# Optimization experiments

Measured on AMD Instinct MI355X. Metric: run time of the kernel, lower is better.

The kernel has to match this reference:

```python
import jax, jax.numpy as jnp
import numpy as np

N_NODES = 50000
N_EDGES = 800000
IN_F = 128
OUT_F = 128

def setup_inputs() -> dict:
    key = jax.random.key(0)
    k1, k2, k3, k4, k5, k6 = jax.random.split(key, 6)
    x = jax.random.normal(k1, (N_NODES, IN_F), dtype=jnp.float32)
    edge_row = jax.random.randint(k2, (N_EDGES,), 0, N_NODES, dtype=jnp.int32)
    edge_col = jax.random.randint(k3, (N_EDGES,), 0, N_NODES, dtype=jnp.int32)
    edge_val = jax.random.uniform(k4, (N_EDGES,), dtype=jnp.float32)
    stdv = 1.0 / np.sqrt(OUT_F)
    weight = jax.random.uniform(k5, (IN_F, OUT_F), minval=-stdv, maxval=stdv, dtype=jnp.float32)
    bias_param = jax.random.uniform(k6, (OUT_F,), minval=-stdv, maxval=stdv, dtype=jnp.float32)
    return {"x": x, "edge_row": edge_row, "edge_col": edge_col,
            "edge_val": edge_val, "weight": weight, "bias_param": bias_param}

def reference(x, edge_row, edge_col, edge_val, weight, bias_param):
    # support = X @ W  (dense GEMM)
    support = jnp.matmul(x, weight)                      # [N, out_f]
    # out = spmm(adj, support): gather source rows, scale by edge value,
    # scatter-add into destination rows (COO SpMM)
    msgs = edge_val[:, None] * support[edge_col]         # [E, out_f]
    out = jax.ops.segment_sum(msgs, edge_row, num_segments=N_NODES)
    return out + bias_param
```

## Files before the change

kernel.cpp:

```cpp
#include <hip/hip_runtime.h>

#define IN_F 128
#define OUT_F 128
#define BROWS 64
#define BCAP  2048
#define NBMAX 1024

typedef __attribute__((ext_vector_type(8))) short short8;
typedef __attribute__((ext_vector_type(4))) float floatx4;

__device__ __forceinline__ short f2bf(float f) {
  union { float f; unsigned u; } v; v.f = f;
  unsigned u = v.u;
  unsigned r = (u + 0x7fffu + ((u >> 16) & 1u)) >> 16;
  return (short)r;
}
__device__ __forceinline__ float bflo(unsigned u) { return __uint_as_float(u << 16); }
__device__ __forceinline__ float bfhi(unsigned u) { return __uint_as_float(u & 0xffff0000u); }

__global__ __launch_bounds__(256) void prep_wt(const float* __restrict__ w,
                                               short* __restrict__ wt) {
  int i = blockIdx.x * 256 + threadIdx.x;
  int n = i >> 7, k = i & 127;
  wt[i] = f2bf(w[k * 128 + n]);
}

__global__ __launch_bounds__(256) void gemm_mfma(const float* __restrict__ x,
                                                 const short* __restrict__ wt,
                                                 unsigned short* __restrict__ sup,
                                                 int n) {
  const int w    = threadIdx.x >> 6;
  const int lane = threadIdx.x & 63;
  const int m    = lane & 15;
  const int q    = lane >> 4;
  const int row  = blockIdx.x * 64 + w * 16 + m;

  floatx4 acc[8];
#pragma unroll
  for (int t = 0; t < 8; ++t) acc[t] = (floatx4)(0.f);

#pragma unroll
  for (int kk = 0; kk < 4; ++kk) {
    short8 a;
    if (row < n) {
      const float4* px = (const float4*)(x + (size_t)row * IN_F + kk * 32 + q * 8);
      float4 lo = px[0], hi = px[1];
      a[0] = f2bf(lo.x); a[1] = f2bf(lo.y); a[2] = f2bf(lo.z); a[3] = f2bf(lo.w);
      a[4] = f2bf(hi.x); a[5] = f2bf(hi.y); a[6] = f2bf(hi.z); a[7] = f2bf(hi.w);
    } else {
      a = (short8)(0);
    }
#pragma unroll
    for (int t = 0; t < 8; ++t) {
      short8 b = *(const short8*)(wt + (size_t)(16 * t + m) * 128 + kk * 32 + q * 8);
      acc[t] = __builtin_amdgcn_mfma_f32_16x16x32_bf16(a, b, acc[t], 0, 0, 0);
    }
  }

#pragma unroll
  for (int r = 0; r < 4; ++r) {
    int row_out = blockIdx.x * 64 + w * 16 + q * 4 + r;
    if (row_out < n) {
#pragma unroll
      for (int t = 0; t < 8; ++t) {
        sup[(size_t)row_out * OUT_F + 16 * t + m] = (unsigned short)f2bf(acc[t][r]);
      }
    }
  }
}

__global__ __launch_bounds__(256) void init_cursor(int* __restrict__ cursor, int nb) {
  int b = blockIdx.x * 256 + threadIdx.x;
  if (b < nb) cursor[b] = b * BCAP;
}

__global__ __launch_bounds__(256) void bin_edges(const int* __restrict__ erow,
                                                 const int* __restrict__ ecol,
                                                 const float* __restrict__ eval_,
                                                 int* __restrict__ cursor,
                                                 int2* __restrict__ slab,
                                                 int n_edges, int nb) {
  __shared__ int lhist[NBMAX];
  const int t = threadIdx.x;
  for (int b = t; b < nb; b += 256) lhist[b] = 0;
  __syncthreads();

  const int base = blockIdx.x * 4096;
  int meta[16], col[16]; float val[16];
#pragma unroll
  for (int i = 0; i < 16; ++i) {
    int e = base + i * 256 + t;
    meta[i] = -1;
    if (e < n_edges) {
      int r  = erow[e];
      col[i] = ecol[e];
      val[i] = eval_[e];
      int b = r >> 6, rl = r & 63;
      int rank = atomicAdd(&lhist[b], 1);
      meta[i] = (b << 18) | (rl << 12) | rank;
    }
  }
  __syncthreads();

  for (int b = t; b < nb; b += 256) {
    int c = lhist[b];
    lhist[b] = c ? atomicAdd(&cursor[b], c) : 0;
  }
  __syncthreads();

#pragma unroll
  for (int i = 0; i < 16; ++i) {
    if (meta[i] >= 0) {
      int b = meta[i] >> 18, rl = (meta[i] >> 12) & 63, rank = meta[i] & 0xfff;
      int pos = lhist[b] + rank;
      if (pos < (b + 1) * BCAP)
        slab[pos] = make_int2(col[i] | (rl << 16), __float_as_int(val[i]));
    }
  }
}

__global__ __launch_bounds__(256) void spmm_sorted(const int* __restrict__ cursor,
                                                   const int2* __restrict__ slab,
                                                   const uint4* __restrict__ supv,
                                                   const float* __restrict__ bias,
                                                   float* __restrict__ out,
                                                   int n_nodes) {
  __shared__ int2 srec[BCAP];
  __shared__ int  roff[BROWS + 1];
  __shared__ int  rcur[BROWS];
  const int t = threadIdx.x, b = blockIdx.x;
  const int start = b * BCAP;
  const int cnt = min(cursor[b] - start, BCAP);
  const int w = t >> 6, lane = t & 63;

  if (t < BROWS) rcur[t] = 0;
  __syncthreads();
  for (int i = t; i < cnt; i += 256)
    atomicAdd(&rcur[(slab[start + i].x >> 16) & 63], 1);
  __syncthreads();
  if (w == 0) {
    int inc = rcur[lane];
    #pragma unroll
    for (int d = 1; d < 64; d <<= 1) {
      int u = __shfl_up(inc, d);
      if (lane >= d) inc += u;
    }
    roff[lane + 1] = inc;
    if (lane == 0) roff[0] = 0;
  }
  __syncthreads();
  if (t < BROWS) rcur[t] = roff[t];
  __syncthreads();
  for (int i = t; i < cnt; i += 256) {
    int2 r = slab[start + i];
    int p = atomicAdd(&rcur[(r.x >> 16) & 63], 1);
    srec[p] = r;
  }
  __syncthreads();

  const int g = lane >> 4, s = lane & 15;
  const float4* bp = (const float4*)bias + s * 2;
  const float4 b0 = bp[0], b1 = bp[1];

  for (int it = 0; it < 4; ++it) {
    const int rl = w * 16 + it * 4 + g;
    const int s0 = roff[rl];
    const int c  = roff[rl + 1] - s0;
    int mx = max(c, __shfl_xor(c, 16));
    mx = max(mx, __shfl_xor(mx, 32));

    float a0 = 0.f, a1 = 0.f, a2 = 0.f, a3 = 0.f,
          a4 = 0.f, a5 = 0.f, a6 = 0.f, a7 = 0.f;

    int2 rec0 = make_int2(0, 0), rec1 = make_int2(0, 0);
    if (0 < c) rec0 = srec[s0];
    if (1 < c) rec1 = srec[s0 + 1];
    uint4 sv0 = supv[(size_t)(rec0.x & 0xffff) * 16 + s];
    uint4 sv1 = supv[(size_t)(rec1.x & 0xffff) * 16 + s];

    for (int j = 0; j < mx; ++j) {
      int2 rec2 = make_int2(0, 0);
      if (j + 2 < c) rec2 = srec[s0 + j + 2];
      uint4 sv2 = supv[(size_t)(rec2.x & 0xffff) * 16 + s];
      float v = (j < c) ? __int_as_float(rec0.y) : 0.f;
      a0 = fmaf(v, bflo(sv0.x), a0);
      a1 = fmaf(v, bfhi(sv0.x), a1);
      a2 = fmaf(v, bflo(sv0.y), a2);
      a3 = fmaf(v, bfhi(sv0.y), a3);
      a4 = fmaf(v, bflo(sv0.z), a4);
      a5 = fmaf(v, bfhi(sv0.z), a5);
      a6 = fmaf(v, bflo(sv0.w), a6);
      a7 = fmaf(v, bfhi(sv0.w), a7);
      rec0 = rec1; rec1 = rec2; sv0 = sv1; sv1 = sv2;
    }

    const int row = b * BROWS + rl;
    if (row < n_nodes) {
      float4* op = (float4*)(out + (size_t)row * OUT_F + s * 8);
      op[0] = make_float4(a0 + b0.x, a1 + b0.y, a2 + b0.z, a3 + b0.w);
      op[1] = make_float4(a4 + b1.x, a5 + b1.y, a6 + b1.z, a7 + b1.w);
    }
  }
}

extern "C" void kernel_launch(void* const* d_in, const int* in_sizes, int n_in,
                              void* d_out, int out_size, void* d_ws, size_t ws_size,
                              hipStream_t stream) {
  const float* x     = (const float*)d_in[0];
  const int*   erow  = (const int*)d_in[1];
  const int*   ecol  = (const int*)d_in[2];
  const float* eval_ = (const float*)d_in[3];
  const float* w     = (const float*)d_in[4];
  const float* bias  = (const float*)d_in[5];
  float* out = (float*)d_out;

  const int n_nodes = in_sizes[0] / IN_F;
  const int n_edges = in_sizes[1];
  const int nb = (n_nodes + BROWS - 1) / BROWS;

  char* ws = (char*)d_ws;
  size_t off = 0;
  auto carve = [&](size_t bytes) { void* p = ws + off; off = (off + bytes + 255) & ~(size_t)255; return p; };
  unsigned short* sup = (unsigned short*)carve((size_t)n_nodes * OUT_F * sizeof(unsigned short));
  short* wt           = (short*)carve((size_t)IN_F * OUT_F * sizeof(short));
  int*   cursor       = (int*)  carve((size_t)nb * sizeof(int));
  int2*  slab         = (int2*) carve((size_t)nb * BCAP * sizeof(int2));

  prep_wt<<<(IN_F * OUT_F) / 256, 256, 0, stream>>>(w, wt);
  gemm_mfma<<<(n_nodes + 63) / 64, 256, 0, stream>>>(x, wt, sup, n_nodes);
  init_cursor<<<(nb + 255) / 256, 256, 0, stream>>>(cursor, nb);
  bin_edges<<<(n_edges + 4095) / 4096, 256, 0, stream>>>(erow, ecol, eval_, cursor, slab,
                                                         n_edges, nb);
  spmm_sorted<<<nb, 256, 0, stream>>>(cursor, slab, (const uint4*)sup, bias, out, n_nodes);
}
```

Measured before the change: 152.0 us.

## Fuse all stages into one persistent cooperative kernel with grid syncs

Merges weight prep, GEMM, cursor init, edge binning and SpMM into a single cooperative persistent kernel separated by grid.sync. The GEMM tiles and edge-binning chunks run concurrently in one work loop. Row buckets shrink to 32 rows with a smaller per-bucket capacity and 2048-edge chunks. This removes several kernel launches and lets the GEMM overlap with binning. In exchange it adds grid-wide barriers, extra shared-memory use from the combined buffers that may lower occupancy, and a tighter bucket capacity (mean about 512 edges per bucket, cap 768) that could overflow and silently drop edges.

```diff
diff --git a/kernel.cpp b/kernel.cpp
--- a/kernel.cpp
+++ b/kernel.cpp
@@ -1,10 +1,14 @@
 #include <hip/hip_runtime.h>
+#include <hip/hip_cooperative_groups.h>
+
+namespace cg = cooperative_groups;
 
 #define IN_F 128
 #define OUT_F 128
-#define BROWS 64
-#define BCAP  2048
-#define NBMAX 1024
+#define BROWS 32
+#define BCAP  768
+#define CHUNK 2048
+#define NBMAX 2048
 
 typedef __attribute__((ext_vector_type(8))) short short8;
 typedef __attribute__((ext_vector_type(4))) float floatx4;
@@ -18,188 +22,184 @@
 __device__ __forceinline__ float bflo(unsigned u) { return __uint_as_float(u << 16); }
 __device__ __forceinline__ float bfhi(unsigned u) { return __uint_as_float(u & 0xffff0000u); }
 
-__global__ __launch_bounds__(256) void prep_wt(const float* __restrict__ w,
-                                               short* __restrict__ wt) {
-  int i = blockIdx.x * 256 + threadIdx.x;
-  int n = i >> 7, k = i & 127;
-  wt[i] = f2bf(w[k * 128 + n]);
-}
-
-__global__ __launch_bounds__(256) void gemm_mfma(const float* __restrict__ x,
-                                                 const short* __restrict__ wt,
-                                                 unsigned short* __restrict__ sup,
-                                                 int n) {
-  const int w    = threadIdx.x >> 6;
-  const int lane = threadIdx.x & 63;
-  const int m    = lane & 15;
-  const int q    = lane >> 4;
-  const int row  = blockIdx.x * 64 + w * 16 + m;
-
-  floatx4 acc[8];
-#pragma unroll
-  for (int t = 0; t < 8; ++t) acc[t] = (floatx4)(0.f);
-
-#pragma unroll
-  for (int kk = 0; kk < 4; ++kk) {
-    short8 a;
-    if (row < n) {
-      const float4* px = (const float4*)(x + (size_t)row * IN_F + kk * 32 + q * 8);
-      float4 lo = px[0], hi = px[1];
-      a[0] = f2bf(lo.x); a[1] = f2bf(lo.y); a[2] = f2bf(lo.z); a[3] = f2bf(lo.w);
-      a[4] = f2bf(hi.x); a[5] = f2bf(hi.y); a[6] = f2bf(hi.z); a[7] = f2bf(hi.w);
-    } else {
-      a = (short8)(0);
-    }
-#pragma unroll
-    for (int t = 0; t < 8; ++t) {
-      short8 b = *(const short8*)(wt + (size_t)(16 * t + m) * 128 + kk * 32 + q * 8);
-      acc[t] = __builtin_amdgcn_mfma_f32_16x16x32_bf16(a, b, acc[t], 0, 0, 0);
-    }
-  }
-
-#pragma unroll
-  for (int r = 0; r < 4; ++r) {
-    int row_out = blockIdx.x * 64 + w * 16 + q * 4 + r;
-    if (row_out < n) {
-#pragma unroll
-      for (int t = 0; t < 8; ++t) {
-        sup[(size_t)row_out * OUT_F + 16 * t + m] = (unsigned short)f2bf(acc[t][r]);
-      }
-    }
-  }
-}
-
-__global__ __launch_bounds__(256) void init_cursor(int* __restrict__ cursor, int nb) {
-  int b = blockIdx.x * 256 + threadIdx.x;
-  if (b < nb) cursor[b] = b * BCAP;
-}
-
-__global__ __launch_bounds__(256) void bin_edges(const int* __restrict__ erow,
-                                                 const int* __restrict__ ecol,
-                                                 const float* __restrict__ eval_,
-                                                 int* __restrict__ cursor,
-                                                 int2* __restrict__ slab,
-                                                 int n_edges, int nb) {
-  __shared__ int lhist[NBMAX];
-  const int t = threadIdx.x;
-  for (int b = t; b < nb; b += 256) lhist[b] = 0;
-  __syncthreads();
-
-  const int base = blockIdx.x * 4096;
-  int meta[16], col[16]; float val[16];
-#pragma unroll
-  for (int i = 0; i < 16; ++i) {
-    int e = base + i * 256 + t;
-    meta[i] = -1;
-    if (e < n_edges) {
-      int r  = erow[e];
-      col[i] = ecol[e];
-      val[i] = eval_[e];
-      int b = r >> 6, rl = r & 63;
-      int rank = atomicAdd(&lhist[b], 1);
-      meta[i] = (b << 18) | (rl << 12) | rank;
-    }
-  }
-  __syncthreads();
-
-  for (int b = t; b < nb; b += 256) {
-    int c = lhist[b];
-    lhist[b] = c ? atomicAdd(&cursor[b], c) : 0;
-  }
-  __syncthreads();
-
-#pragma unroll
-  for (int i = 0; i < 16; ++i) {
-    if (meta[i] >= 0) {
-      int b = meta[i] >> 18, rl = (meta[i] >> 12) & 63, rank = meta[i] & 0xfff;
-      int pos = lhist[b] + rank;
-      if (pos < (b + 1) * BCAP)
-        slab[pos] = make_int2(col[i] | (rl << 16), __float_as_int(val[i]));
-    }
-  }
-}
-
-__global__ __launch_bounds__(256) void spmm_sorted(const int* __restrict__ cursor,
-                                                   const int2* __restrict__ slab,
-                                                   const uint4* __restrict__ supv,
-                                                   const float* __restrict__ bias,
-                                                   float* __restrict__ out,
-                                                   int n_nodes) {
+__global__ void fused(const float* __restrict__ x,
+                      const int* __restrict__ erow,
+                      const int* __restrict__ ecol,
+                      const float* __restrict__ eval_,
+                      const float* __restrict__ w,
+                      const float* __restrict__ bias,
+                      short* __restrict__ wt,
+                      int* __restrict__ cursor,
+                      int2* __restrict__ slab,
+                      unsigned short* __restrict__ sup,
+                      float* __restrict__ out,
+                      int n_nodes, int n_edges, int nb, int n_tiles, int n_chunks) {
+  __shared__ int  lhist[NBMAX];
   __shared__ int2 srec[BCAP];
   __shared__ int  roff[BROWS + 1];
   __shared__ int  rcur[BROWS];
-  const int t = threadIdx.x, b = blockIdx.x;
-  const int start = b * BCAP;
-  const int cnt = min(cursor[b] - start, BCAP);
-  const int w = t >> 6, lane = t & 63;
-
-  if (t < BROWS) rcur[t] = 0;
-  __syncthreads();
-  for (int i = t; i < cnt; i += 256)
-    atomicAdd(&rcur[(slab[start + i].x >> 16) & 63], 1);
-  __syncthreads();
-  if (w == 0) {
-    int inc = rcur[lane];
-    #pragma unroll
-    for (int d = 1; d < 64; d <<= 1) {
-      int u = __shfl_up(inc, d);
-      if (lane >= d) inc += u;
-    }
-    roff[lane + 1] = inc;
-    if (lane == 0) roff[0] = 0;
+  cg::grid_group grid = cg::this_grid();
+  const int t = threadIdx.x;
+  const int wv = t >> 6, lane = t & 63;
+  const int G = gridDim.x;
+
+  for (int i = blockIdx.x * 256 + t; i < IN_F * OUT_F; i += G * 256) {
+    int nn = i >> 7, k = i & 127;
+    wt[i] = f2bf(w[k * OUT_F + nn]);
   }
-  __syncthreads();
-  if (t < BROWS) rcur[t] = roff[t];
-  __syncthreads();
-  for (int i = t; i < cnt; i += 256) {
-    int2 r = slab[start + i];
-    int p = atomicAdd(&rcur[(r.x >> 16) & 63], 1);
-    srec[p] = r;
+  for (int i = blockIdx.x * 256 + t; i < nb; i += G * 256) cursor[i] = i * BCAP;
+  grid.sync();
+
+  for (int u = blockIdx.x; u < n_tiles + n_chunks; u += G) {
+    if (u < n_tiles) {
+      const int m = lane & 15, q = lane >> 4;
+      const int row = u * 64 + wv * 16 + m;
+#pragma unroll
+      for (int half = 0; half < 2; ++half) {
+        floatx4 acc[4];
+#pragma unroll
+        for (int i2 = 0; i2 < 4; ++i2) acc[i2] = (floatx4)(0.f);
+#pragma unroll
+        for (int kk = 0; kk < 4; ++kk) {
+          short8 a;
+          if (row < n_nodes) {
+            const float4* px = (const float4*)(x + (size_t)row * IN_F + kk * 32 + q * 8);
+            float4 lo = px[0], hi = px[1];
+            a[0] = f2bf(lo.x); a[1] = f2bf(lo.y); a[2] = f2bf(lo.z); a[3] = f2bf(lo.w);
+            a[4] = f2bf(hi.x); a[5] = f2bf(hi.y); a[6] = f2bf(hi.z); a[7] = f2bf(hi.w);
+          } else {
+            a = (short8)(0);
+          }
+#pragma unroll
+          for (int t4 = 0; t4 < 4; ++t4) {
+            int ncol = half * 64 + 16 * t4 + m;
+            short8 bfr = *(const short8*)(wt + (size_t)ncol * IN_F + kk * 32 + q * 8);
+            acc[t4] = __builtin_amdgcn_mfma_f32_16x16x32_bf16(a, bfr, acc[t4], 0, 0, 0);
+          }
+        }
+#pragma unroll
+        for (int r = 0; r < 4; ++r) {
+          int row_out = u * 64 + wv * 16 + q * 4 + r;
+          if (row_out < n_nodes) {
+#pragma unroll
+            for (int t4 = 0; t4 < 4; ++t4)
+              sup[(size_t)row_out * OUT_F + half * 64 + 16 * t4 + m] =
+                  (unsigned short)f2bf(acc[t4][r]);
+          }
+        }
+      }
+    } else {
+      const int C = u - n_tiles;
+      for (int i = t; i < nb; i += 256) lhist[i] = 0;
+      __syncthreads();
+      const int base = C * CHUNK;
+      int meta[CHUNK / 256]; int col8[CHUNK / 256]; float val8[CHUNK / 256];
+#pragma unroll
+      for (int i = 0; i < CHUNK / 256; ++i) {
+        int e = base + i * 256 + t;
+        meta[i] = -1;
+        if (e < n_edges) {
+          int r  = erow[e];
+          col8[i] = ecol[e];
+          val8[i] = eval_[e];
+          int bk = r >> 5, rl = r & 31;
+          int rank = atomicAdd(&lhist[bk], 1);
+          meta[i] = (bk << 16) | (rl << 11) | rank;
+        }
+      }
+      __syncthreads();
+      for (int bk = t; bk < nb; bk += 256) {
+        int c = lhist[bk];
+        lhist[bk] = c ? atomicAdd(&cursor[bk], c) : 0;
+      }
+      __syncthreads();
+#pragma unroll
+      for (int i = 0; i < CHUNK / 256; ++i) {
+        if (meta[i] >= 0) {
+          int bk = meta[i] >> 16, rl = (meta[i] >> 11) & 31, rank = meta[i] & 0x7ff;
+          int pos = lhist[bk] + rank;
+          if (pos < (bk + 1) * BCAP)
+            slab[pos] = make_int2(col8[i] | (rl << 16), __float_as_int(val8[i]));
+        }
+      }
+      __syncthreads();
+    }
   }
-  __syncthreads();
-
+  grid.sync();
+
+  const uint4* supv = (const uint4*)sup;
   const int g = lane >> 4, s = lane & 15;
   const float4* bp = (const float4*)bias + s * 2;
   const float4 b0 = bp[0], b1 = bp[1];
 
-  for (int it = 0; it < 4; ++it) {
-    const int rl = w * 16 + it * 4 + g;
-    const int s0 = roff[rl];
-    const int c  = roff[rl + 1] - s0;
-    int mx = max(c, __shfl_xor(c, 16));
-    mx = max(mx, __shfl_xor(mx, 32));
-
-    float a0 = 0.f, a1 = 0.f, a2 = 0.f, a3 = 0.f,
-          a4 = 0.f, a5 = 0.f, a6 = 0.f, a7 = 0.f;
-
-    int2 rec0 = make_int2(0, 0), rec1 = make_int2(0, 0);
-    if (0 < c) rec0 = srec[s0];
-    if (1 < c) rec1 = srec[s0 + 1];
-    uint4 sv0 = supv[(size_t)(rec0.x & 0xffff) * 16 + s];
-    uint4 sv1 = supv[(size_t)(rec1.x & 0xffff) * 16 + s];
-
-    for (int j = 0; j < mx; ++j) {
-      int2 rec2 = make_int2(0, 0);
-      if (j + 2 < c) rec2 = srec[s0 + j + 2];
-      uint4 sv2 = supv[(size_t)(rec2.x & 0xffff) * 16 + s];
-      float v = (j < c) ? __int_as_float(rec0.y) : 0.f;
-      a0 = fmaf(v, bflo(sv0.x), a0);
-      a1 = fmaf(v, bfhi(sv0.x), a1);
-      a2 = fmaf(v, bflo(sv0.y), a2);
-      a3 = fmaf(v, bfhi(sv0.y), a3);
-      a4 = fmaf(v, bflo(sv0.z), a4);
-      a5 = fmaf(v, bfhi(sv0.z), a5);
-      a6 = fmaf(v, bflo(sv0.w), a6);
-      a7 = fmaf(v, bfhi(sv0.w), a7);
-      rec0 = rec1; rec1 = rec2; sv0 = sv1; sv1 = sv2;
-    }
-
-    const int row = b * BROWS + rl;
-    if (row < n_nodes) {
-      float4* op = (float4*)(out + (size_t)row * OUT_F + s * 8);
-      op[0] = make_float4(a0 + b0.x, a1 + b0.y, a2 + b0.z, a3 + b0.w);
-      op[1] = make_float4(a4 + b1.x, a5 + b1.y, a6 + b1.z, a7 + b1.w);
-    }
+  for (int bk = blockIdx.x; bk < nb; bk += G) {
+    if (t < BROWS) rcur[t] = 0;
+    __syncthreads();
+    const int start = bk * BCAP;
+    const int cnt = min(cursor[bk] - start, BCAP);
+    for (int i = t; i < cnt; i += 256)
+      atomicAdd(&rcur[(slab[start + i].x >> 16) & 31], 1);
+    __syncthreads();
+    if (wv == 0) {
+      int c = (lane < BROWS) ? rcur[lane] : 0;
+      int inc = c;
+#pragma unroll
+      for (int d = 1; d < BROWS; d <<= 1) {
+        int u2 = __shfl_up(inc, d);
+        if (lane >= d) inc += u2;
+      }
+      if (lane < BROWS) roff[lane + 1] = inc;
+      if (lane == 0) roff[0] = 0;
+    }
+    __syncthreads();
+    if (t < BROWS) rcur[t] = roff[t];
+    __syncthreads();
+    for (int i = t; i < cnt; i += 256) {
+      int2 r = slab[start + i];
+      int p = atomicAdd(&rcur[(r.x >> 16) & 31], 1);
+      srec[p] = r;
+    }
+    __syncthreads();
+#pragma unroll
+    for (int it = 0; it < 2; ++it) {
+      const int rl = it * 16 + wv * 4 + g;
+      const int s0 = roff[rl];
+      const int c  = roff[rl + 1] - s0;
+      int mx = max(c, __shfl_xor(c, 16));
+      mx = max(mx, __shfl_xor(mx, 32));
+
+      float a0 = 0.f, a1 = 0.f, a2 = 0.f, a3 = 0.f,
+            a4 = 0.f, a5 = 0.f, a6 = 0.f, a7 = 0.f;
+      int2 rec0 = make_int2(0, 0), rec1 = make_int2(0, 0);
+      if (0 < c) rec0 = srec[s0];
+      if (1 < c) rec1 = srec[s0 + 1];
+      uint4 sv0 = supv[(size_t)(rec0.x & 0xffff) * 16 + s];
+      uint4 sv1 = supv[(size_t)(rec1.x & 0xffff) * 16 + s];
+
+      for (int j = 0; j < mx; ++j) {
+        int2 rec2 = make_int2(0, 0);
+        if (j + 2 < c) rec2 = srec[s0 + j + 2];
+        uint4 sv2 = supv[(size_t)(rec2.x & 0xffff) * 16 + s];
+        float v = (j < c) ? __int_as_float(rec0.y) : 0.f;
+        a0 = fmaf(v, bflo(sv0.x), a0);
+        a1 = fmaf(v, bfhi(sv0.x), a1);
+        a2 = fmaf(v, bflo(sv0.y), a2);
+        a3 = fmaf(v, bfhi(sv0.y), a3);
+        a4 = fmaf(v, bflo(sv0.z), a4);
+        a5 = fmaf(v, bfhi(sv0.z), a5);
+        a6 = fmaf(v, bflo(sv0.w), a6);
+        a7 = fmaf(v, bfhi(sv0.w), a7);
+        rec0 = rec1; rec1 = rec2; sv0 = sv1; sv1 = sv2;
+      }
+
+      const int row = bk * BROWS + rl;
+      if (row < n_nodes) {
+        float4* op = (float4*)(out + (size_t)row * OUT_F + s * 8);
+        op[0] = make_float4(a0 + b0.x, a1 + b0.y, a2 + b0.z, a3 + b0.w);
+        op[1] = make_float4(a4 + b1.x, a5 + b1.y, a6 + b1.z, a7 + b1.w);
+      }
+    }
+    __syncthreads();
   }
 }
 
@@ -214,9 +214,11 @@
   const float* bias  = (const float*)d_in[5];
   float* out = (float*)d_out;
 
-  const int n_nodes = in_sizes[0] / IN_F;
-  const int n_edges = in_sizes[1];
-  const int nb = (n_nodes + BROWS - 1) / BROWS;
+  int n_nodes  = in_sizes[0] / IN_F;
+  int n_edges  = in_sizes[1];
+  int nb       = (n_nodes + BROWS - 1) / BROWS;
+  int n_tiles  = (n_nodes + 63) / 64;
+  int n_chunks = (n_edges + CHUNK - 1) / CHUNK;
 
   char* ws = (char*)d_ws;
   size_t off = 0;
@@ -226,10 +228,17 @@
   int*   cursor       = (int*)  carve((size_t)nb * sizeof(int));
   int2*  slab         = (int2*) carve((size_t)nb * BCAP * sizeof(int2));
 
-  prep_wt<<<(IN_F * OUT_F) / 256, 256, 0, stream>>>(w, wt);
-  gemm_mfma<<<(n_nodes + 63) / 64, 256, 0, stream>>>(x, wt, sup, n_nodes);
-  init_cursor<<<(nb + 255) / 256, 256, 0, stream>>>(cursor, nb);
-  bin_edges<<<(n_edges + 4095) / 4096, 256, 0, stream>>>(erow, ecol, eval_, cursor, slab,
-                                                         n_edges, nb);
-  spmm_sorted<<<nb, 256, 0, stream>>>(cursor, slab, (const uint4*)sup, bias, out, n_nodes);
+  int maxB = 0;
+  (void)hipOccupancyMaxActiveBlocksPerMultiprocessor(&maxB, fused, 256, 0);
+  if (maxB < 1) maxB = 1;
+  if (maxB > 8) maxB = 8;
+  int grid = 256 * maxB;
+
+  void* args[] = { (void*)&x, (void*)&erow, (void*)&ecol, (void*)&eval_,
+                   (void*)&w, (void*)&bias, (void*)&wt, (void*)&cursor,
+                   (void*)&slab, (void*)&sup, (void*)&out,
+                   (void*)&n_nodes, (void*)&n_edges, (void*)&nb,
+                   (void*)&n_tiles, (void*)&n_chunks };
+  (void)hipLaunchCooperativeKernel((const void*)fused, dim3(grid), dim3(256),
+                                   args, 0, stream);
 }
```

After: 293.0 us. 92.8% more time.

## Fuse GEMM with edge binning in one launch and halve bucket size

Applied to the files above, without the earlier changes.

Merges the MFMA GEMM and the edge-binning kernel into one grid, where the leading blocks do GEMM tiles and the rest bin edge chunks, so the two independent phases overlap. Cursor init moves into the weight-prep kernel, cutting the launch count from five to three. Buckets shrink from 64 to 32 rows, which doubles the SpMM block count, and binning blocks now handle 8192 edges while reloading row, col and val instead of keeping them in registers. The SpMM stages the slab in shared memory once, so it reads global memory once instead of twice. Risks are a higher bucket-overflow chance with the smaller capacity and extra global reloads in binning.

```diff
diff --git a/kernel.cpp b/kernel.cpp
--- a/kernel.cpp
+++ b/kernel.cpp
@@ -2,9 +2,10 @@
 
 #define IN_F 128
 #define OUT_F 128
-#define BROWS 64
-#define BCAP  2048
-#define NBMAX 1024
+#define BROWS 32
+#define BCAP  1024
+#define CHUNK 8192
+#define NBMAX 2048
 
 typedef __attribute__((ext_vector_type(8))) short short8;
 typedef __attribute__((ext_vector_type(4))) float floatx4;
@@ -18,103 +19,93 @@
 __device__ __forceinline__ float bflo(unsigned u) { return __uint_as_float(u << 16); }
 __device__ __forceinline__ float bfhi(unsigned u) { return __uint_as_float(u & 0xffff0000u); }
 
-__global__ __launch_bounds__(256) void prep_wt(const float* __restrict__ w,
-                                               short* __restrict__ wt) {
+__global__ __launch_bounds__(256) void prep_all(const float* __restrict__ w,
+                                                short* __restrict__ wt,
+                                                int* __restrict__ cursor, int nb) {
   int i = blockIdx.x * 256 + threadIdx.x;
   int n = i >> 7, k = i & 127;
   wt[i] = f2bf(w[k * 128 + n]);
-}
-
-__global__ __launch_bounds__(256) void gemm_mfma(const float* __restrict__ x,
-                                                 const short* __restrict__ wt,
-                                                 unsigned short* __restrict__ sup,
-                                                 int n) {
-  const int w    = threadIdx.x >> 6;
-  const int lane = threadIdx.x & 63;
-  const int m    = lane & 15;
-  const int q    = lane >> 4;
-  const int row  = blockIdx.x * 64 + w * 16 + m;
-
-  floatx4 acc[8];
-#pragma unroll
-  for (int t = 0; t < 8; ++t) acc[t] = (floatx4)(0.f);
-
-#pragma unroll
-  for (int kk = 0; kk < 4; ++kk) {
-    short8 a;
-    if (row < n) {
-      const float4* px = (const float4*)(x + (size_t)row * IN_F + kk * 32 + q * 8);
-      float4 lo = px[0], hi = px[1];
-      a[0] = f2bf(lo.x); a[1] = f2bf(lo.y); a[2] = f2bf(lo.z); a[3] = f2bf(lo.w);
-      a[4] = f2bf(hi.x); a[5] = f2bf(hi.y); a[6] = f2bf(hi.z); a[7] = f2bf(hi.w);
-    } else {
-      a = (short8)(0);
-    }
-#pragma unroll
-    for (int t = 0; t < 8; ++t) {
-      short8 b = *(const short8*)(wt + (size_t)(16 * t + m) * 128 + kk * 32 + q * 8);
-      acc[t] = __builtin_amdgcn_mfma_f32_16x16x32_bf16(a, b, acc[t], 0, 0, 0);
-    }
-  }
-
-#pragma unroll
-  for (int r = 0; r < 4; ++r) {
-    int row_out = blockIdx.x * 64 + w * 16 + q * 4 + r;
-    if (row_out < n) {
-#pragma unroll
-      for (int t = 0; t < 8; ++t) {
-        sup[(size_t)row_out * OUT_F + 16 * t + m] = (unsigned short)f2bf(acc[t][r]);
-      }
-    }
-  }
-}
-
-__global__ __launch_bounds__(256) void init_cursor(int* __restrict__ cursor, int nb) {
-  int b = blockIdx.x * 256 + threadIdx.x;
-  if (b < nb) cursor[b] = b * BCAP;
-}
-
-__global__ __launch_bounds__(256) void bin_edges(const int* __restrict__ erow,
-                                                 const int* __restrict__ ecol,
-                                                 const float* __restrict__ eval_,
-                                                 int* __restrict__ cursor,
-                                                 int2* __restrict__ slab,
-                                                 int n_edges, int nb) {
+  if (i < nb) cursor[i] = i * BCAP;
+}
+
+__global__ __launch_bounds__(256) void gemm_bin(const float* __restrict__ x,
+                                                const short* __restrict__ wt,
+                                                unsigned short* __restrict__ sup,
+                                                const int* __restrict__ erow,
+                                                const int* __restrict__ ecol,
+                                                const float* __restrict__ eval_,
+                                                int* __restrict__ cursor,
+                                                int2* __restrict__ slab,
+                                                int n_nodes, int n_edges,
+                                                int nb, int n_tiles) {
   __shared__ int lhist[NBMAX];
   const int t = threadIdx.x;
-  for (int b = t; b < nb; b += 256) lhist[b] = 0;
-  __syncthreads();
-
-  const int base = blockIdx.x * 4096;
-  int meta[16], col[16]; float val[16];
-#pragma unroll
-  for (int i = 0; i < 16; ++i) {
-    int e = base + i * 256 + t;
-    meta[i] = -1;
-    if (e < n_edges) {
-      int r  = erow[e];
-      col[i] = ecol[e];
-      val[i] = eval_[e];
-      int b = r >> 6, rl = r & 63;
-      int rank = atomicAdd(&lhist[b], 1);
-      meta[i] = (b << 18) | (rl << 12) | rank;
-    }
-  }
-  __syncthreads();
-
-  for (int b = t; b < nb; b += 256) {
-    int c = lhist[b];
-    lhist[b] = c ? atomicAdd(&cursor[b], c) : 0;
-  }
-  __syncthreads();
-
-#pragma unroll
-  for (int i = 0; i < 16; ++i) {
-    if (meta[i] >= 0) {
-      int b = meta[i] >> 18, rl = (meta[i] >> 12) & 63, rank = meta[i] & 0xfff;
-      int pos = lhist[b] + rank;
-      if (pos < (b + 1) * BCAP)
-        slab[pos] = make_int2(col[i] | (rl << 16), __float_as_int(val[i]));
+
+  if ((int)blockIdx.x < n_tiles) {
+    const int wv   = t >> 6;
+    const int lane = t & 63;
+    const int m    = lane & 15;
+    const int q    = lane >> 4;
+    const int row  = blockIdx.x * 64 + wv * 16 + m;
+
+    floatx4 acc[8];
+#pragma unroll
+    for (int k = 0; k < 8; ++k) acc[k] = (floatx4)(0.f);
+
+#pragma unroll
+    for (int kk = 0; kk < 4; ++kk) {
+      short8 a;
+      if (row < n_nodes) {
+        const float4* px = (const float4*)(x + (size_t)row * IN_F + kk * 32 + q * 8);
+        float4 lo = px[0], hi = px[1];
+        a[0] = f2bf(lo.x); a[1] = f2bf(lo.y); a[2] = f2bf(lo.z); a[3] = f2bf(lo.w);
+        a[4] = f2bf(hi.x); a[5] = f2bf(hi.y); a[6] = f2bf(hi.z); a[7] = f2bf(hi.w);
+      } else {
+        a = (short8)(0);
+      }
+#pragma unroll
+      for (int k = 0; k < 8; ++k) {
+        short8 b = *(const short8*)(wt + (size_t)(16 * k + m) * 128 + kk * 32 + q * 8);
+        acc[k] = __builtin_amdgcn_mfma_f32_16x16x32_bf16(a, b, acc[k], 0, 0, 0);
+      }
+    }
+#pragma unroll
+    for (int r = 0; r < 4; ++r) {
+      int row_out = blockIdx.x * 64 + wv * 16 + q * 4 + r;
+      if (row_out < n_nodes) {
+#pragma unroll
+        for (int k = 0; k < 8; ++k)
+          sup[(size_t)row_out * OUT_F + 16 * k + m] = (unsigned short)f2bf(acc[k][r]);
+      }
+    }
+  } else {
+    for (int b = t; b < nb; b += 256) lhist[b] = 0;
+    __syncthreads();
+
+    const int base = (blockIdx.x - n_tiles) * CHUNK;
+    int rank[CHUNK / 256];
+#pragma unroll
+    for (int i = 0; i < CHUNK / 256; ++i) {
+      int e = base + i * 256 + t;
+      rank[i] = -1;
+      if (e < n_edges) rank[i] = atomicAdd(&lhist[erow[e] >> 5], 1);
+    }
+    __syncthreads();
+    for (int b = t; b < nb; b += 256) {
+      int c = lhist[b];
+      lhist[b] = c ? atomicAdd(&cursor[b], c) : 0;
+    }
+    __syncthreads();
+#pragma unroll
+    for (int i = 0; i < CHUNK / 256; ++i) {
+      if (rank[i] >= 0) {
+        int e = base + i * 256 + t;
+        int r = erow[e];
+        int bk = r >> 5, rl = r & 31;
+        int pos = lhist[bk] + rank[i];
+        if (pos < (bk + 1) * BCAP)
+          slab[pos] = make_int2(ecol[e] | (rl << 16), __float_as_int(eval_[e]));
+      }
     }
   }
 }
@@ -125,36 +116,41 @@
                                                    const float* __restrict__ bias,
                                                    float* __restrict__ out,
                                                    int n_nodes) {
-  __shared__ int2 srec[BCAP];
+  __shared__ int2 sin[BCAP];
+  __shared__ int2 sout[BCAP];
   __shared__ int  roff[BROWS + 1];
   __shared__ int  rcur[BROWS];
   const int t = threadIdx.x, b = blockIdx.x;
   const int start = b * BCAP;
   const int cnt = min(cursor[b] - start, BCAP);
-  const int w = t >> 6, lane = t & 63;
+  const int wv = t >> 6, lane = t & 63;
 
   if (t < BROWS) rcur[t] = 0;
   __syncthreads();
-  for (int i = t; i < cnt; i += 256)
-    atomicAdd(&rcur[(slab[start + i].x >> 16) & 63], 1);
-  __syncthreads();
-  if (w == 0) {
-    int inc = rcur[lane];
-    #pragma unroll
-    for (int d = 1; d < 64; d <<= 1) {
+  for (int i = t; i < cnt; i += 256) {
+    int2 r = slab[start + i];
+    sin[i] = r;
+    atomicAdd(&rcur[(r.x >> 16) & 31], 1);
+  }
+  __syncthreads();
+  if (wv == 0) {
+    int c = (lane < BROWS) ? rcur[lane] : 0;
+    int inc = c;
+#pragma unroll
+    for (int d = 1; d < BROWS; d <<= 1) {
       int u = __shfl_up(inc, d);
       if (lane >= d) inc += u;
     }
-    roff[lane + 1] = inc;
+    if (lane < BROWS) roff[lane + 1] = inc;
     if (lane == 0) roff[0] = 0;
   }
   __syncthreads();
   if (t < BROWS) rcur[t] = roff[t];
   __syncthreads();
   for (int i = t; i < cnt; i += 256) {
-    int2 r = slab[start + i];
-    int p = atomicAdd(&rcur[(r.x >> 16) & 63], 1);
-    srec[p] = r;
+    int2 r = sin[i];
+    int p = atomicAdd(&rcur[(r.x >> 16) & 31], 1);
+    sout[p] = r;
   }
   __syncthreads();
 
@@ -162,8 +158,9 @@
   const float4* bp = (const float4*)bias + s * 2;
   const float4 b0 = bp[0], b1 = bp[1];
 
-  for (int it = 0; it < 4; ++it) {
-    const int rl = w * 16 + it * 4 + g;
+#pragma unroll
+  for (int it = 0; it < 2; ++it) {
+    const int rl = it * 16 + wv * 4 + g;
     const int s0 = roff[rl];
     const int c  = roff[rl + 1] - s0;
     int mx = max(c, __shfl_xor(c, 16));
@@ -173,14 +170,14 @@
           a4 = 0.f, a5 = 0.f, a6 = 0.f, a7 = 0.f;
 
     int2 rec0 = make_int2(0, 0), rec1 = make_int2(0, 0);
-    if (0 < c) rec0 = srec[s0];
-    if (1 < c) rec1 = srec[s0 + 1];
+    if (0 < c) rec0 = sout[s0];
+    if (1 < c) rec1 = sout[s0 + 1];
     uint4 sv0 = supv[(size_t)(rec0.x & 0xffff) * 16 + s];
     uint4 sv1 = supv[(size_t)(rec1.x & 0xffff) * 16 + s];
 
     for (int j = 0; j < mx; ++j) {
       int2 rec2 = make_int2(0, 0);
-      if (j + 2 < c) rec2 = srec[s0 + j + 2];
+      if (j + 2 < c) rec2 = sout[s0 + j + 2];
       uint4 sv2 = supv[(size_t)(rec2.x & 0xffff) * 16 + s];
       float v = (j < c) ? __int_as_float(rec0.y) : 0.f;
       a0 = fmaf(v, bflo(sv0.x), a0);
@@ -214,9 +211,11 @@
   const float* bias  = (const float*)d_in[5];
   float* out = (float*)d_out;
 
-  const int n_nodes = in_sizes[0] / IN_F;
-  const int n_edges = in_sizes[1];
-  const int nb = (n_nodes + BROWS - 1) / BROWS;
+  const int n_nodes  = in_sizes[0] / IN_F;
+  const int n_edges  = in_sizes[1];
+  const int nb       = (n_nodes + BROWS - 1) / BROWS;
+  const int n_tiles  = (n_nodes + 63) / 64;
+  const int n_chunks = (n_edges + CHUNK - 1) / CHUNK;
 
   char* ws = (char*)d_ws;
   size_t off = 0;
@@ -226,10 +225,9 @@
   int*   cursor       = (int*)  carve((size_t)nb * sizeof(int));
   int2*  slab         = (int2*) carve((size_t)nb * BCAP * sizeof(int2));
 
-  prep_wt<<<(IN_F * OUT_F) / 256, 256, 0, stream>>>(w, wt);
-  gemm_mfma<<<(n_nodes + 63) / 64, 256, 0, stream>>>(x, wt, sup, n_nodes);
-  init_cursor<<<(nb + 255) / 256, 256, 0, stream>>>(cursor, nb);
-  bin_edges<<<(n_edges + 4095) / 4096, 256, 0, stream>>>(erow, ecol, eval_, cursor, slab,
-                                                         n_edges, nb);
+  prep_all<<<64, 256, 0, stream>>>(w, wt, cursor, nb);
+  gemm_bin<<<n_tiles + n_chunks, 256, 0, stream>>>(x, wt, sup, erow, ecol, eval_,
+                                                   cursor, slab, n_nodes, n_edges,
+                                                   nb, n_tiles);
   spmm_sorted<<<nb, 256, 0, stream>>>(cursor, slab, (const uint4*)sup, bias, out, n_nodes);
 }
```

Measured after the change: 177.4 us. 16.7% more time.
